# Kernel optimization log

Hardware: AMD Instinct MI355X
Metric: run time of the kernel (lower is better)

Reference implementation:

```python
import jax, jax.numpy as jnp
import numpy as np

NUM_CLASSES = 80
NUM_ANCHORS = 3
# anchors [12,16,19,36,40,28] / stride 8, masked by [0,1,2]
ANCHOR_W = np.array([1.5, 2.375, 5.0], dtype=np.float32)
ANCHOR_H = np.array([2.0, 4.5, 3.5], dtype=np.float32)


def setup_inputs() -> dict:
    key = jax.random.key(0)
    output = jax.random.normal(key, (32, (5 + NUM_CLASSES) * NUM_ANCHORS, 76, 76), dtype=jnp.float32)
    return {"output": output}


def reference(output):
    B, Ctot, H, W = output.shape
    A, C = NUM_ANCHORS, NUM_CLASSES
    # [B, A, 5+C, H, W]
    o = output.reshape(B, A, 5 + C, H, W)

    bxy = jax.nn.sigmoid(o[:, :, 0:2])          # [B, A, 2, H, W]
    bwh = jnp.exp(o[:, :, 2:4])                  # [B, A, 2, H, W]
    det = jax.nn.sigmoid(o[:, :, 4])             # [B, A, H, W]
    cls = jax.nn.softmax(o[:, :, 5:], axis=2)    # softmax over class dim -> [B, A, C, H, W]

    grid_x = jnp.arange(W, dtype=output.dtype)[None, None, None, :]   # broadcast over H
    grid_y = jnp.arange(H, dtype=output.dtype)[None, None, :, None]   # broadcast over W
    aw = jnp.asarray(ANCHOR_W, dtype=output.dtype)[None, :, None, None]
    ah = jnp.asarray(ANCHOR_H, dtype=output.dtype)[None, :, None, None]

    bx = (bxy[:, :, 0] + grid_x) / W             # [B, A, H, W]
    by = (bxy[:, :, 1] + grid_y) / H
    bw = bwh[:, :, 0] * aw / W
    bh = bwh[:, :, 1] * ah / H

    boxes = jnp.stack([bx, by, bw, bh], axis=-1).reshape(B, A * H * W, 4)
    # cls: [B, A, C, H, W] -> [B, A, H, W, C] -> [B, A*H*W, C] (matches permute(0,1,3,2) on HW-flat)
    cls_confs = jnp.transpose(cls, (0, 1, 3, 4, 2)).reshape(B, A * H * W, C)
    det_confs = det.reshape(B, A * H * W, 1)
    confs = cls_confs * det_confs
    return (boxes, confs)
```

## Files before the change

kernel.cpp:

```cpp
#include <hip/hip_runtime.h>

#define NUM_CLASSES 80
#define NUM_ANCHORS 3
#define GRID_HW 76
#define HWSZ (GRID_HW * GRID_HW)
#define BATCH 32
#define CH_PER_A (5 + NUM_CLASSES)
#define TOTAL (BATCH * NUM_ANCHORS * HWSZ)
#define ROWPAD 81

__constant__ float c_aw[3] = {1.5f, 2.375f, 5.0f};
__constant__ float c_ah[3] = {2.0f, 4.5f, 3.5f};

__global__ __launch_bounds__(256) void yolo_kernel(
    const float* __restrict__ in, float* __restrict__ out)
{
    __shared__ float lds[4][16][ROWPAD];

    const int tid  = threadIdx.x;
    const int wv   = tid >> 6;
    const int lane = tid & 63;
    const int lq   = lane & 3;
    const int lr   = lane >> 2;

    const int loc = blockIdx.x * 64 + wv * 16 + lr;
    const int hw  = loc % HWSZ;
    const int ba  = loc / HWSZ;
    const int a   = ba % NUM_ANCHORS;
    const int gx  = hw % GRID_HW;
    const int gy  = hw / GRID_HW;
    const size_t base = (size_t)ba * (CH_PER_A * HWSZ) + hw;

    const float inv = 1.0f / (float)GRID_HW;

    {
        float t = in[base + (size_t)lq * HWSZ];
        float bval;
        if (lq == 0)      bval = ((float)gx + 1.0f / (1.0f + __expf(-t))) * inv;
        else if (lq == 1) bval = ((float)gy + 1.0f / (1.0f + __expf(-t))) * inv;
        else if (lq == 2) bval = __expf(t) * c_aw[a] * inv;
        else              bval = __expf(t) * c_ah[a] * inv;
        out[(size_t)loc * 4 + lq] = bval;
    }

    float det = 0.0f;
    if (lq == 0) {
        float td = in[base + (size_t)4 * HWSZ];
        det = 1.0f / (1.0f + __expf(-td));
    }
    det = __shfl(det, lane & ~3);

    float s = 0.0f;
    const int c0 = lq * 20;
#pragma unroll
    for (int cc = 0; cc < 20; ++cc) {
        float x = in[base + (size_t)(5 + c0 + cc) * HWSZ];
        float e = __expf(x);
        s += e;
        lds[wv][lr][c0 + cc] = e;
    }
    s += __shfl_xor(s, 1);
    s += __shfl_xor(s, 2);
    const float scale = det / s;
    if (lq == 0) lds[wv][lr][80] = scale;

    __syncthreads();

    const size_t conf_base = (size_t)TOTAL * 4 +
        ((size_t)blockIdx.x * 64 + wv * 16) * NUM_CLASSES;
    float2* co = (float2*)(out + conf_base);
#pragma unroll
    for (int j = 0; j < 10; ++j) {
        int g   = j * 64 + lane;
        int f   = g * 2;
        int lr2 = f / 80;
        int c   = f % 80;
        float sc = lds[wv][lr2][80];
        co[g] = make_float2(lds[wv][lr2][c] * sc, lds[wv][lr2][c + 1] * sc);
    }
}

extern "C" void kernel_launch(void* const* d_in, const int* in_sizes, int n_in,
                              void* d_out, int out_size, void* d_ws, size_t ws_size,
                              hipStream_t stream) {
    const float* in = (const float*)d_in[0];
    float* out = (float*)d_out;
    const int block = 256;
    const int grid = TOTAL / 64;
    yolo_kernel<<<grid, block, 0, stream>>>(in, out);
}
```

Before: 75.27 us.

## Vectorize class loads as float4 per 4 locations, widen stores, use nontemporal writes

Class logits are now read as float4 vectors covering 4 consecutive spatial locations per thread, exponentiated and written transposed into a shared tile. Softmax sums are then computed from LDS. Confidence output is written as float4 with nontemporal stores, and box output also uses nontemporal stores. The intent is fewer, wider global memory transactions and less cache pollution from write-once outputs, at the cost of an extra barrier and LDS bank traffic on the transposed writes. The float4 loads assume groups of 4 locations never straddle a batch-anchor boundary, which holds because 5776 is divisible by 4.

```diff
diff --git a/kernel.cpp b/kernel.cpp
--- a/kernel.cpp
+++ b/kernel.cpp
@@ -7,76 +7,102 @@
 #define BATCH 32
 #define CH_PER_A (5 + NUM_CLASSES)
 #define TOTAL (BATCH * NUM_ANCHORS * HWSZ)
-#define ROWPAD 81
+#define P 81
+
+typedef float v4f __attribute__((ext_vector_type(4)));
 
 __constant__ float c_aw[3] = {1.5f, 2.375f, 5.0f};
 __constant__ float c_ah[3] = {2.0f, 4.5f, 3.5f};
 
-__global__ __launch_bounds__(256) void yolo_kernel(
-    const float* __restrict__ in, float* __restrict__ out)
+__global__ __launch_bounds__(256) void yolo_kernel(const float* __restrict__ in,
+                                                   float* __restrict__ out)
 {
-    __shared__ float lds[4][16][ROWPAD];
+    __shared__ float lds_e[64][P];
 
-    const int tid  = threadIdx.x;
-    const int wv   = tid >> 6;
-    const int lane = tid & 63;
-    const int lq   = lane & 3;
-    const int lr   = lane >> 2;
-
-    const int loc = blockIdx.x * 64 + wv * 16 + lr;
-    const int hw  = loc % HWSZ;
-    const int ba  = loc / HWSZ;
-    const int a   = ba % NUM_ANCHORS;
-    const int gx  = hw % GRID_HW;
-    const int gy  = hw / GRID_HW;
-    const size_t base = (size_t)ba * (CH_PER_A * HWSZ) + hw;
-
-    const float inv = 1.0f / (float)GRID_HW;
+    const int tid = threadIdx.x;
+    const int blk = blockIdx.x;
 
     {
-        float t = in[base + (size_t)lq * HWSZ];
+        const int grp = tid & 15;
+        const int chq = tid >> 4;
+        const int loc4 = blk * 64 + grp * 4;
+        const int hw4  = loc4 % HWSZ;
+        const int ba4  = loc4 / HWSZ;
+        const float* inb = in + (size_t)ba4 * (CH_PER_A * HWSZ)
+                              + (size_t)5 * HWSZ + hw4;
+        const int l0 = grp * 4;
+#pragma unroll
+        for (int j = 0; j < 5; ++j) {
+            const int ch = j * 16 + chq;
+            const v4f x = *(const v4f*)(inb + (size_t)ch * HWSZ);
+            lds_e[l0 + 0][ch] = __expf(x.x);
+            lds_e[l0 + 1][ch] = __expf(x.y);
+            lds_e[l0 + 2][ch] = __expf(x.z);
+            lds_e[l0 + 3][ch] = __expf(x.w);
+        }
+    }
+    __syncthreads();
+
+    const int wv = tid >> 6, lane = tid & 63;
+    const int lq = lane & 3, lr = lane >> 2;
+    const int l  = wv * 16 + lr;
+    const int loc = blk * 64 + l;
+    {
+        const int hw = loc % HWSZ;
+        const int ba = loc / HWSZ;
+        const int a  = ba % NUM_ANCHORS;
+        const int gx = hw % GRID_HW, gy = hw / GRID_HW;
+        const size_t base = (size_t)ba * (CH_PER_A * HWSZ) + hw;
+        const float inv = 1.0f / (float)GRID_HW;
+
+        const int c0 = lq * 20;
+        float s0 = 0.f, s1 = 0.f, s2 = 0.f, s3 = 0.f;
+#pragma unroll
+        for (int cc = 0; cc < 20; cc += 4) {
+            s0 += lds_e[l][c0 + cc + 0];
+            s1 += lds_e[l][c0 + cc + 1];
+            s2 += lds_e[l][c0 + cc + 2];
+            s3 += lds_e[l][c0 + cc + 3];
+        }
+        float s = (s0 + s1) + (s2 + s3);
+        s += __shfl_xor(s, 1);
+        s += __shfl_xor(s, 2);
+
+        const float t = in[base + (size_t)lq * HWSZ];
         float bval;
         if (lq == 0)      bval = ((float)gx + 1.0f / (1.0f + __expf(-t))) * inv;
         else if (lq == 1) bval = ((float)gy + 1.0f / (1.0f + __expf(-t))) * inv;
         else if (lq == 2) bval = __expf(t) * c_aw[a] * inv;
         else              bval = __expf(t) * c_ah[a] * inv;
-        out[(size_t)loc * 4 + lq] = bval;
+        __builtin_nontemporal_store(bval, out + (size_t)loc * 4 + lq);
+
+        float det = 0.0f;
+        if (lq == 0) {
+            const float td = in[base + (size_t)4 * HWSZ];
+            det = 1.0f / (1.0f + __expf(-td));
+        }
+        det = __shfl(det, lane & ~3);
+        if (lq == 0) lds_e[l][80] = det / s;
     }
-
-    float det = 0.0f;
-    if (lq == 0) {
-        float td = in[base + (size_t)4 * HWSZ];
-        det = 1.0f / (1.0f + __expf(-td));
-    }
-    det = __shfl(det, lane & ~3);
-
-    float s = 0.0f;
-    const int c0 = lq * 20;
-#pragma unroll
-    for (int cc = 0; cc < 20; ++cc) {
-        float x = in[base + (size_t)(5 + c0 + cc) * HWSZ];
-        float e = __expf(x);
-        s += e;
-        lds[wv][lr][c0 + cc] = e;
-    }
-    s += __shfl_xor(s, 1);
-    s += __shfl_xor(s, 2);
-    const float scale = det / s;
-    if (lq == 0) lds[wv][lr][80] = scale;
-
     __syncthreads();
 
-    const size_t conf_base = (size_t)TOTAL * 4 +
-        ((size_t)blockIdx.x * 64 + wv * 16) * NUM_CLASSES;
-    float2* co = (float2*)(out + conf_base);
+    {
+        float* cout = out + (size_t)TOTAL * 4
+                    + ((size_t)blk * 64 + wv * 16) * NUM_CLASSES;
 #pragma unroll
-    for (int j = 0; j < 10; ++j) {
-        int g   = j * 64 + lane;
-        int f   = g * 2;
-        int lr2 = f / 80;
-        int c   = f % 80;
-        float sc = lds[wv][lr2][80];
-        co[g] = make_float2(lds[wv][lr2][c] * sc, lds[wv][lr2][c + 1] * sc);
+        for (int j = 0; j < 5; ++j) {
+            const int g  = j * 64 + lane;
+            const int ll = g / 20;
+            const int c4 = (g % 20) * 4;
+            const int li = wv * 16 + ll;
+            const float sc = lds_e[li][80];
+            v4f o;
+            o.x = lds_e[li][c4 + 0] * sc;
+            o.y = lds_e[li][c4 + 1] * sc;
+            o.z = lds_e[li][c4 + 2] * sc;
+            o.w = lds_e[li][c4 + 3] * sc;
+            __builtin_nontemporal_store(o, (v4f*)(cout + (size_t)ll * 80 + c4));
+        }
     }
 }
 
```

Measured after the change: 64.95 us. 1.16x faster.

## Remap lanes to class-by-location, vectorize loads, drop LDS transpose

Applied to the files above, without the earlier changes.

Each wave now assigns lanes as 16 class slots by 4 groups of 4 locations. Class logits are loaded as float4 along the spatial dimension, and the softmax sum is reduced with cross-lane shuffles, which removes the LDS staging buffer and the __syncthreads. Reciprocals now use the fast rcp intrinsic, and outputs go through nontemporal stores. In exchange, the confs stores become scattered 4-byte writes with an 80-float stride rather than contiguous float2 writes, which may hurt write coalescing.

```diff
diff --git a/kernel.cpp b/kernel.cpp
--- a/kernel.cpp
+++ b/kernel.cpp
@@ -7,76 +7,78 @@
 #define BATCH 32
 #define CH_PER_A (5 + NUM_CLASSES)
 #define TOTAL (BATCH * NUM_ANCHORS * HWSZ)
-#define ROWPAD 81
+
+typedef float v4f __attribute__((ext_vector_type(4)));
 
 __constant__ float c_aw[3] = {1.5f, 2.375f, 5.0f};
 __constant__ float c_ah[3] = {2.0f, 4.5f, 3.5f};
 
-__global__ __launch_bounds__(256) void yolo_kernel(
-    const float* __restrict__ in, float* __restrict__ out)
+__device__ __forceinline__ float fast_rcp(float x) { return __builtin_amdgcn_rcpf(x); }
+__device__ __forceinline__ float sigmoidf(float x) { return fast_rcp(1.0f + __expf(-x)); }
+
+__global__ __launch_bounds__(256) void yolo_kernel(const float* __restrict__ in,
+                                                   float* __restrict__ out)
 {
-    __shared__ float lds[4][16][ROWPAD];
-
     const int tid  = threadIdx.x;
     const int wv   = tid >> 6;
     const int lane = tid & 63;
-    const int lq   = lane & 3;
-    const int lr   = lane >> 2;
+    const int c    = lane >> 2;
+    const int g    = lane & 3;
 
-    const int loc = blockIdx.x * 64 + wv * 16 + lr;
-    const int hw  = loc % HWSZ;
-    const int ba  = loc / HWSZ;
-    const int a   = ba % NUM_ANCHORS;
-    const int gx  = hw % GRID_HW;
-    const int gy  = hw / GRID_HW;
-    const size_t base = (size_t)ba * (CH_PER_A * HWSZ) + hw;
-
+    const int locbase = blockIdx.x * 64 + wv * 16;
+    const int hwb = locbase % HWSZ;
+    const int ba  = locbase / HWSZ;
+    const int a   = ba - (ba / 3) * 3;
+    const float* inb = in + (size_t)ba * (CH_PER_A * HWSZ);
     const float inv = 1.0f / (float)GRID_HW;
 
-    {
-        float t = in[base + (size_t)lq * HWSZ];
-        float bval;
-        if (lq == 0)      bval = ((float)gx + 1.0f / (1.0f + __expf(-t))) * inv;
-        else if (lq == 1) bval = ((float)gy + 1.0f / (1.0f + __expf(-t))) * inv;
-        else if (lq == 2) bval = __expf(t) * c_aw[a] * inv;
-        else              bval = __expf(t) * c_ah[a] * inv;
-        out[(size_t)loc * 4 + lq] = bval;
+    float e[5][4];
+    float p0 = 0.f, p1 = 0.f, p2 = 0.f, p3 = 0.f;
+#pragma unroll
+    for (int j = 0; j < 5; ++j) {
+        const v4f x = *(const v4f*)(inb + (size_t)(5 + c + 16 * j) * HWSZ + hwb + g * 4);
+        e[j][0] = __expf(x.x); e[j][1] = __expf(x.y);
+        e[j][2] = __expf(x.z); e[j][3] = __expf(x.w);
+        p0 += e[j][0]; p1 += e[j][1]; p2 += e[j][2]; p3 += e[j][3];
+    }
+#pragma unroll
+    for (int m = 4; m < 64; m <<= 1) {
+        p0 += __shfl_xor(p0, m);
+        p1 += __shfl_xor(p1, m);
+        p2 += __shfl_xor(p2, m);
+        p3 += __shfl_xor(p3, m);
+    }
+    const v4f dt = *(const v4f*)(inb + (size_t)4 * HWSZ + hwb + g * 4);
+    float sc[4];
+    sc[0] = sigmoidf(dt.x) * fast_rcp(p0);
+    sc[1] = sigmoidf(dt.y) * fast_rcp(p1);
+    sc[2] = sigmoidf(dt.z) * fast_rcp(p2);
+    sc[3] = sigmoidf(dt.w) * fast_rcp(p3);
+
+    float* cout = out + (size_t)TOTAL * 4 + (size_t)locbase * NUM_CLASSES;
+#pragma unroll
+    for (int j = 0; j < 5; ++j) {
+#pragma unroll
+        for (int k = 0; k < 4; ++k) {
+            __builtin_nontemporal_store(e[j][k] * sc[k],
+                cout + (size_t)(g * 4 + k) * NUM_CLASSES + c + 16 * j);
+        }
     }
 
-    float det = 0.0f;
-    if (lq == 0) {
-        float td = in[base + (size_t)4 * HWSZ];
-        det = 1.0f / (1.0f + __expf(-td));
-    }
-    det = __shfl(det, lane & ~3);
+    {
+        const int hw  = hwb + c;
+        const int gyb = hwb / GRID_HW;
+        const int rem = hwb - gyb * GRID_HW;
+        int gx = rem + c, gy = gyb;
+        if (gx >= GRID_HW) { gx -= GRID_HW; gy += 1; }
 
-    float s = 0.0f;
-    const int c0 = lq * 20;
-#pragma unroll
-    for (int cc = 0; cc < 20; ++cc) {
-        float x = in[base + (size_t)(5 + c0 + cc) * HWSZ];
-        float e = __expf(x);
-        s += e;
-        lds[wv][lr][c0 + cc] = e;
-    }
-    s += __shfl_xor(s, 1);
-    s += __shfl_xor(s, 2);
-    const float scale = det / s;
-    if (lq == 0) lds[wv][lr][80] = scale;
-
-    __syncthreads();
-
-    const size_t conf_base = (size_t)TOTAL * 4 +
-        ((size_t)blockIdx.x * 64 + wv * 16) * NUM_CLASSES;
-    float2* co = (float2*)(out + conf_base);
-#pragma unroll
-    for (int j = 0; j < 10; ++j) {
-        int g   = j * 64 + lane;
-        int f   = g * 2;
-        int lr2 = f / 80;
-        int c   = f % 80;
-        float sc = lds[wv][lr2][80];
-        co[g] = make_float2(lds[wv][lr2][c] * sc, lds[wv][lr2][c + 1] * sc);
+        const float t = inb[(size_t)g * HWSZ + hw];
+        float bval;
+        if (g == 0)      bval = ((float)gx + sigmoidf(t)) * inv;
+        else if (g == 1) bval = ((float)gy + sigmoidf(t)) * inv;
+        else if (g == 2) bval = __expf(t) * c_aw[a] * inv;
+        else             bval = __expf(t) * c_ah[a] * inv;
+        __builtin_nontemporal_store(bval, out + (size_t)locbase * 4 + lane);
     }
 }
 
```

Result: slower. 80.19 us (+6.5%).
